# Kernel optimization log

Measured on AMD Instinct MI355X. Metric: run time of the kernel, lower is better.

The kernel has to match this reference:

```python
import jax, jax.numpy as jnp
import numpy as np
from jax import lax

P = 8      # patch size (SGU hard-codes 8x8)
K = 7      # dynamic depthwise kernel size
EPS = 1e-5

def _gelu(x):
    return jax.nn.gelu(x, approximate=False)

def _ln_last(x, w, b):
    mu = jnp.mean(x, -1, keepdims=True)
    var = jnp.var(x, -1, keepdims=True)
    return (x - mu) / jnp.sqrt(var + EPS) * w + b

def _ln_chan(x, w, b):
    # WithBias LayerNorm over channel dim of an NCHW tensor (to_3d/to_4d)
    mu = jnp.mean(x, 1, keepdims=True)
    var = jnp.var(x, 1, keepdims=True)
    return (x - mu) / jnp.sqrt(var + EPS) * w[:, None, None] + b[:, None, None]

def _c1(x, w, b=None):
    # 1x1 conv on NCHW; w: (O, C)
    y = jnp.einsum('bchw,oc->bohw', x, w)
    return y if b is None else y + b[:, None, None]

def _dw3(x, w, b):
    # depthwise 3x3, padding 1; w: (C, 3, 3)
    C = x.shape[1]
    y = lax.conv_general_dilated(x, w[:, None], (1, 1), 'SAME',
        feature_group_count=C, dimension_numbers=('NCHW', 'OIHW', 'NCHW'))
    return y + b[:, None, None]

def _idynamic_dw(x, wdyn):
    # content-adaptive depthwise conv: x (B,C,P,P), per-position kernels
    # wdyn (B,K*K,P,P) shared across channels (groups = C // heads = 1)
    pad = K // 2
    xp = jnp.pad(x, ((0, 0), (0, 0), (pad, pad), (pad, pad)))
    out = jnp.zeros_like(x)
    for k in range(K * K):  # fixed small kernel loop, fused under jit
        i, j = divmod(k, K)
        out = out + xp[:, :, i:i + P, j:j + P] * wdyn[:, k][:, None]
    return out

def _forward(x, w_hid, b_hid, xcnn_w1, xcnn_b1, xcnn_ln_w, xcnn_ln_b,
             xcnn_dw_w, xcnn_dw_b, ci_w1, ci_b1, ci_ln_w, ci_ln_b, ci_w2, ci_b2,
             si_w1, si_b1, si_ln_w, si_ln_b, si_w2, si_b2,
             proj_w, proj_b, out_w, out_b, sgu_ln_w, sgu_ln_b,
             dwb_w0, idw_w1, idw_b1, idw_bn_w, idw_bn_b, idw_w2, idw_b2, dwb_w2):
    b, c, h, w = x.shape
    hh, ww = h // P, w // P
    n = hh * ww
    half = c // 2

    x = _gelu(_c1(x, w_hid, b_hid))
    # b c (hh P)(ww P) -> b hh ww p1 p2 c
    xp = x.reshape(b, c, hh, P, ww, P).transpose(0, 2, 4, 3, 5, 1)
    x_seq = xp.reshape(b, n, P * P, c)

    # x_cnn branch on (b*n, c, 8, 8) patch images
    xc = xp.reshape(b * n, P, P, c).transpose(0, 3, 1, 2)
    xc = _c1(xc, xcnn_w1, xcnn_b1)
    xc = _ln_chan(xc, xcnn_ln_w, xcnn_ln_b)
    xc = _gelu(_dw3(xc, xcnn_dw_w, xcnn_dw_b))

    # channel interaction SE gate -> (b*n, c//2, 1, 1)
    pooled = jnp.mean(xc, (2, 3), keepdims=True)
    cdw = _c1(pooled, ci_w1, ci_b1)
    cdw = _gelu(_ln_chan(cdw, ci_ln_w, ci_ln_b))
    cdw = jax.nn.sigmoid(_c1(cdw, ci_w2, ci_b2))

    # SpatialGatingUnit
    res = x_seq[..., :half].reshape(b * n, P * P, half)
    gate = x_seq[..., half:].reshape(b * n, P * P, half)
    gate = gate * cdw.reshape(b * n, 1, half)
    gate = _ln_last(gate, sgu_ln_w, sgu_ln_b)
    g = gate.reshape(b * n, P, P, half).transpose(0, 3, 1, 2)
    g = _c1(g, dwb_w0)
    # IDynamicDWConv kernel generation (1x1 -> BN(eval, stats 0/1) -> ReLU -> 1x1)
    t = _c1(g, idw_w1, idw_b1)
    t = t / jnp.sqrt(1.0 + EPS) * idw_bn_w[:, None, None] + idw_bn_b[:, None, None]
    t = jax.nn.relu(t)
    wdyn = _c1(t, idw_w2, idw_b2)  # (b*n, K*K, 8, 8)
    g = _idynamic_dw(g, wdyn)
    g = _c1(g, dwb_w2)
    gate = g.transpose(0, 2, 3, 1).reshape(b * n, P * P, half)
    x_sgu = gate * res  # act = Identity

    # stitch patches back to full resolution
    xc_full = xc.reshape(b, hh, ww, c, P, P).transpose(0, 3, 1, 4, 2, 5).reshape(b, c, h, w)
    x_att = x_sgu.reshape(b, hh, ww, P, P, half).transpose(0, 5, 1, 3, 2, 4).reshape(b, half, h, w)

    # spatial interaction gate (b,1,h,w)
    si = _c1(x_att, si_w1, si_b1)
    si = _gelu(_ln_chan(si, si_ln_w, si_ln_b))
    si = jax.nn.sigmoid(_c1(si, si_w2, si_b2))

    xproj = _c1(xc_full, proj_w, proj_b) * si
    out = jnp.concatenate([xproj, x_att], axis=1)
    return _c1(out, out_w, out_b)

def setup_inputs() -> dict:
    key = jax.random.key(0)
    ks = iter(jax.random.split(key, 40))
    dim, half = 64, 32
    B, H, W = 4, 256, 256
    def rn(shape):
        fan_in = int(np.prod(shape[1:])) if len(shape) > 1 else int(shape[0])
        return jax.random.normal(next(ks), shape, jnp.float32) / np.sqrt(fan_in)
    z = lambda n: jnp.zeros((n,), jnp.float32)
    o = lambda n: jnp.ones((n,), jnp.float32)
    return {
        'x': jax.random.normal(next(ks), (B, dim, H, W), jnp.float32),
        'w_hid': rn((dim, dim)), 'b_hid': z(dim),
        'xcnn_w1': rn((dim, dim)), 'xcnn_b1': z(dim),
        'xcnn_ln_w': o(dim), 'xcnn_ln_b': z(dim),
        'xcnn_dw_w': rn((dim, 3, 3)), 'xcnn_dw_b': z(dim),
        'ci_w1': rn((dim // 8, dim)), 'ci_b1': z(dim // 8),
        'ci_ln_w': o(dim // 8), 'ci_ln_b': z(dim // 8),
        'ci_w2': rn((half, dim // 8)), 'ci_b2': z(half),
        'si_w1': rn((dim // 16, half)), 'si_b1': z(dim // 16),
        'si_ln_w': o(dim // 16), 'si_ln_b': z(dim // 16),
        'si_w2': rn((1, dim // 16)), 'si_b2': z(1),
        'proj_w': rn((half, dim)), 'proj_b': z(half),
        'out_w': rn((dim, dim)), 'out_b': z(dim),
        'sgu_ln_w': o(half), 'sgu_ln_b': z(half),
        'dwb_w0': rn((half, half)),
        'idw_w1': rn((half // 4, half)), 'idw_b1': z(half // 4),
        'idw_bn_w': o(half // 4), 'idw_bn_b': z(half // 4),
        'idw_w2': rn((K * K, half // 4)), 'idw_b2': z(K * K),
        'dwb_w2': rn((half, half)),
    }

def reference(x, w_hid, b_hid, xcnn_w1, xcnn_b1, xcnn_ln_w, xcnn_ln_b,
              xcnn_dw_w, xcnn_dw_b, ci_w1, ci_b1, ci_ln_w, ci_ln_b, ci_w2, ci_b2,
              si_w1, si_b1, si_ln_w, si_ln_b, si_w2, si_b2,
              proj_w, proj_b, out_w, out_b, sgu_ln_w, sgu_ln_b,
              dwb_w0, idw_w1, idw_b1, idw_bn_w, idw_bn_b, idw_w2, idw_b2, dwb_w2):
    return _forward(x, w_hid, b_hid, xcnn_w1, xcnn_b1, xcnn_ln_w, xcnn_ln_b,
                    xcnn_dw_w, xcnn_dw_b, ci_w1, ci_b1, ci_ln_w, ci_ln_b, ci_w2, ci_b2,
                    si_w1, si_b1, si_ln_w, si_ln_b, si_w2, si_b2,
                    proj_w, proj_b, out_w, out_b, sgu_ln_w, sgu_ln_b,
                    dwb_w0, idw_w1, idw_b1, idw_bn_w, idw_bn_b, idw_w2, idw_b2, dwb_w2)
```

## Files before the change

kernel.cpp:

```cpp
#include <hip/hip_runtime.h>
#include <math.h>

#define HWSZ 65536
#define EPSF 1e-5f
#define PSTR 4680

typedef __attribute__((ext_vector_type(8))) short bf8v;
typedef __attribute__((ext_vector_type(4))) float f4v;
typedef __attribute__((ext_vector_type(4))) unsigned int u4v;
typedef unsigned int uint32;

#define W_HID_OFF   0
#define W_X1_OFF    4096
#define W_PROJ_OFF  8192
#define W_OUT_OFF   10240
#define W_DWB0_OFF  14336
#define W_DWB2_OFF  15360
#define F_DWT   0
#define F_CI1T  576
#define F_CI2T  1088
#define F_IW1T  1344
#define F_SI1T  1600

__device__ __forceinline__ float sigm(float v){ return 1.0f/(1.0f+expf(-v)); }
__device__ __forceinline__ float bl(uint32 u){ return __uint_as_float(u<<16); }
__device__ __forceinline__ float bh(uint32 u){ return __uint_as_float(u & 0xffff0000u); }
__device__ __forceinline__ uint32 pk2(float a, float b){
  uint32 r; asm("v_cvt_pk_bf16_f32 %0, %1, %2" : "=v"(r) : "v"(a), "v"(b)); return r;
}
__device__ __forceinline__ unsigned short bfr(float x){
  uint32 u = __float_as_uint(x); u += 0x7fffu + ((u>>16)&1u); return (unsigned short)(u>>16);
}
__device__ __forceinline__ float rcp_f(float x){ float r; asm("v_rcp_f32 %0, %1" : "=v"(r) : "v"(x)); return r; }
__device__ __forceinline__ float exp2_f(float x){ float r; asm("v_exp_f32 %0, %1" : "=v"(r) : "v"(x)); return r; }

__device__ __attribute__((noinline)) f4v gelu4(f4v v){
  f4v r;
  #pragma unroll
  for (int i=0;i<4;++i){
    float x  = v[i];
    float z  = fabsf(x) * 0.7071067811865476f;
    float t  = rcp_f(fmaf(0.3275911f, z, 1.0f));
    float p  = t*fmaf(t, fmaf(t, fmaf(t, fmaf(t, 1.061405429f, -1.453152027f),
                       1.421413741f), -0.284496736f), 0.254829592f);
    float ex = exp2_f(-(z*z)*1.4426950408889634f);
    float er = fmaf(-p, ex, 1.0f);
    float s  = copysignf(er, x);
    float hx = 0.5f*x;
    r[i] = fmaf(hx, s, hx);
  }
  return r;
}

#define WSYNC() asm volatile("s_waitcnt lgkmcnt(0)" ::: "memory")

__global__ void prep_w(const float* __restrict__ a0, const float* __restrict__ a1,
                       const float* __restrict__ a2, const float* __restrict__ a3,
                       const float* __restrict__ a4, const float* __restrict__ a5,
                       unsigned short* __restrict__ ws){
  int i = blockIdx.x*256 + threadIdx.x;
  if (i >= 16384) return;
  float v;
  if      (i < 4096)  v = a0[i];
  else if (i < 8192)  v = a1[i-4096];
  else if (i < 10240) v = a2[i-8192];
  else if (i < 14336) v = a3[i-10240];
  else if (i < 15360) v = a4[i-14336];
  else                v = a5[i-15360];
  ws[i] = bfr(v);
}

__global__ void prep_t(const float* __restrict__ dw, const float* __restrict__ ci1,
                       const float* __restrict__ ci2, const float* __restrict__ iw1,
                       const float* __restrict__ sw1, float* __restrict__ wf){
  int i = blockIdx.x*256 + threadIdx.x;
  if (i >= 1728) return;
  float v;
  if (i < 576)        { int k=i/64, c=i%64;            v = dw[c*9+k]; }
  else if (i < 1088)  { int j=i-576,  c=j/8, m=j%8;    v = ci1[m*64+c]; }
  else if (i < 1344)  { int j=i-1088, m=j/32, o=j%32;  v = ci2[o*8+m]; }
  else if (i < 1600)  { int j=i-1344, c=j/8, m=j%8;    v = iw1[m*32+c]; }
  else                { int j=i-1600, c=j/4, m=j%4;    v = sw1[m*32+c]; }
  wf[i] = v;
}

__global__ __launch_bounds__(256, 4)
void gmlp_fused(const float* __restrict__ x,
                const float* __restrict__ b_hid,
                const float* __restrict__ xcnn_b1,
                const float* __restrict__ xcnn_ln_w, const float* __restrict__ xcnn_ln_b,
                const float* __restrict__ xcnn_dw_b,
                const float* __restrict__ ci_b1,
                const float* __restrict__ ci_ln_w, const float* __restrict__ ci_ln_b,
                const float* __restrict__ ci_b2,
                const float* __restrict__ si_b1,
                const float* __restrict__ si_ln_w, const float* __restrict__ si_ln_b,
                const float* __restrict__ si_w2,   const float* __restrict__ si_b2,
                const float* __restrict__ proj_b,
                const float* __restrict__ out_b,
                const float* __restrict__ sgu_ln_w, const float* __restrict__ sgu_ln_b,
                const float* __restrict__ idw_b1,
                const float* __restrict__ idw_bn_w, const float* __restrict__ idw_bn_b,
                const float* __restrict__ idw_w2,  const float* __restrict__ idw_b2,
                const unsigned short* __restrict__ wsw,
                float* __restrict__ out)
{
    __shared__ __align__(16) unsigned short bufS[4*PSTR];
    __shared__ __align__(16) float segate_s[4][32];

    const float* wf = (const float*)wsw + 8192;

    const int tx  = threadIdx.x;
    const int wid = tx >> 6;
    const int t   = tx & 63;
    const int l4  = t & 15, g4 = t >> 4;
    const int py  = t >> 3,  px = t & 7;

    const int bid   = blockIdx.x;
    const int strip = bid & 7;
    const int ph    = (bid >> 3) & 31;
    const int bb    = bid >> 8;

    unsigned short* Wp = bufS + wid*PSTR;

    const int ty  = tx >> 5;
    const int txx = tx & 31;
    const int lp  = txx >> 3;
    const int lpx = txx & 7;
    const int yx  = ty*256 + txx;
    const float* xbase = x + (bb*64)*HWSZ + (ph*8)*256 + strip*32;
    unsigned short* ldst = bufS + lp*PSTR + (ty*8 + lpx)*72;

    #pragma unroll 1
    for (int c8 = 0; c8 < 8; ++c8) {
        u4v w;
        #pragma unroll
        for (int j = 0; j < 4; ++j) {
            int c = c8*8 + 2*j;
            float a = __builtin_nontemporal_load(xbase + c*HWSZ + yx);
            float b = __builtin_nontemporal_load(xbase + (c+1)*HWSZ + yx);
            w[j] = pk2(a, b);
        }
        *(u4v*)(ldst + c8*8) = w;
    }
    if (t < 9) *(u4v*)(Wp + 64*72 + t*8) = (u4v){0,0,0,0};
    __syncthreads();

    f4v acc[4][4];
    #pragma unroll
    for (int m = 0; m < 4; ++m)
        #pragma unroll
        for (int n = 0; n < 4; ++n)
            acc[m][n] = (f4v){0.f,0.f,0.f,0.f};
    #pragma unroll 1
    for (int s = 0; s < 2; ++s) {
        bf8v bw[4]; bf8v av[4];
        #pragma unroll
        for (int n = 0; n < 4; ++n) bw[n] = *(const bf8v*)(wsw + W_HID_OFF + (n*16+l4)*64 + s*32 + g4*8);
        #pragma unroll
        for (int m = 0; m < 4; ++m) av[m] = *(const bf8v*)(Wp + (m*16 + l4)*72 + s*32 + g4*8);
        #pragma unroll
        for (int m = 0; m < 4; ++m)
            #pragma unroll
            for (int n = 0; n < 4; ++n)
                acc[m][n] = __builtin_amdgcn_mfma_f32_16x16x32_bf16(av[m], bw[n], acc[m][n], 0,0,0);
    }
    {
        float bhid[4];
        #pragma unroll
        for (int n = 0; n < 4; ++n) bhid[n] = b_hid[n*16 + l4];
        #pragma unroll
        for (int m = 0; m < 4; ++m)
            #pragma unroll
            for (int n = 0; n < 4; ++n) {
                f4v q;
                #pragma unroll
                for (int r = 0; r < 4; ++r) q[r] = acc[m][n][r] + bhid[n];
                acc[m][n] = gelu4(q);
            }
    }
    WSYNC();
    #pragma unroll
    for (int m = 0; m < 4; ++m)
        #pragma unroll
        for (int n = 0; n < 4; ++n)
            #pragma unroll
            for (int r = 0; r < 4; ++r)
                Wp[(m*16 + g4*4 + r)*72 + n*16 + l4] = bfr(acc[m][n][r]);
    WSYNC();

    uint32 hidpk[32];
    #pragma unroll
    for (int q8 = 0; q8 < 8; ++q8) {
        u4v v = *(const u4v*)(Wp + t*72 + q8*8);
        #pragma unroll
        for (int j = 0; j < 4; ++j) hidpk[q8*4 + j] = v[j];
    }

    #pragma unroll
    for (int m = 0; m < 4; ++m)
        #pragma unroll
        for (int n = 0; n < 4; ++n)
            acc[m][n] = (f4v){0.f,0.f,0.f,0.f};
    #pragma unroll 1
    for (int s = 0; s < 2; ++s) {
        bf8v bw[4]; bf8v av[4];
        #pragma unroll
        for (int n = 0; n < 4; ++n) bw[n] = *(const bf8v*)(wsw + W_X1_OFF + (n*16+l4)*64 + s*32 + g4*8);
        #pragma unroll
        for (int m = 0; m < 4; ++m) av[m] = *(const bf8v*)(Wp + (m*16 + l4)*72 + s*32 + g4*8);
        #pragma unroll
        for (int m = 0; m < 4; ++m)
            #pragma unroll
            for (int n = 0; n < 4; ++n)
                acc[m][n] = __builtin_amdgcn_mfma_f32_16x16x32_bf16(av[m], bw[n], acc[m][n], 0,0,0);
    }
    {
        float bx[4];
        #pragma unroll
        for (int n = 0; n < 4; ++n) bx[n] = xcnn_b1[n*16 + l4];
        #pragma unroll
        for (int m = 0; m < 4; ++m)
            #pragma unroll
            for (int n = 0; n < 4; ++n)
                #pragma unroll
                for (int r = 0; r < 4; ++r)
                    acc[m][n][r] += bx[n];
    }
    WSYNC();
    #pragma unroll
    for (int m = 0; m < 4; ++m)
        #pragma unroll
        for (int n = 0; n < 4; ++n)
            #pragma unroll
            for (int r = 0; r < 4; ++r)
                Wp[(m*16 + g4*4 + r)*72 + n*16 + l4] = bfr(acc[m][n][r]);
    WSYNC();
    {
        float s = 0.f;
        #pragma unroll 1
        for (int q8 = 0; q8 < 8; ++q8) {
            u4v v = *(const u4v*)(Wp + t*72 + q8*8);
            #pragma unroll
            for (int j = 0; j < 4; ++j) s += bl(v[j]) + bh(v[j]);
        }
        float mu = s * (1.f/64.f);
        float s2 = 0.f;
        #pragma unroll 1
        for (int q8 = 0; q8 < 8; ++q8) {
            u4v v = *(const u4v*)(Wp + t*72 + q8*8);
            #pragma unroll
            for (int j = 0; j < 4; ++j) {
                float d0 = bl(v[j]) - mu, d1 = bh(v[j]) - mu;
                s2 = fmaf(d0, d0, fmaf(d1, d1, s2));
            }
        }
        float rstd = rsqrtf(s2*(1.f/64.f) + EPSF);
        #pragma unroll 1
        for (int q8 = 0; q8 < 8; ++q8) {
            u4v v = *(const u4v*)(Wp + t*72 + q8*8);
            u4v w;
            #pragma unroll
            for (int j = 0; j < 4; ++j) {
                int c = q8*8 + 2*j;
                float a = (bl(v[j]) - mu)*rstd*xcnn_ln_w[c]   + xcnn_ln_b[c];
                float b = (bh(v[j]) - mu)*rstd*xcnn_ln_w[c+1] + xcnn_ln_b[c+1];
                w[j] = pk2(a, b);
            }
            *(u4v*)(Wp + t*72 + q8*8) = w;
        }
    }
    WSYNC();

    #pragma unroll 1
    for (int h = 0; h < 2; ++h) {
        float xh[32];
        #pragma unroll
        for (int o = 0; o < 32; ++o) xh[o] = xcnn_dw_b[h*32 + o];
        #pragma unroll 1
        for (int ki = 0; ki < 3; ++ki) {
            #pragma unroll 1
            for (int kj = 0; kj < 3; ++kj) {
                int rr = py + ki - 1, cc = px + kj - 1;
                bool val = ((unsigned)rr < 8u) && ((unsigned)cc < 8u);
                int pnn = val ? rr*8 + cc : 64;
                const unsigned short* rp = Wp + pnn*72 + h*32;
                const float* wp = wf + F_DWT + (ki*3+kj)*64 + h*32;
                #pragma unroll
                for (int c8 = 0; c8 < 4; ++c8) {
                    u4v v = *(const u4v*)(rp + c8*8);
                    #pragma unroll
                    for (int j = 0; j < 4; ++j) {
                        int c = c8*8 + 2*j;
                        xh[c]   = fmaf(bl(v[j]), wp[c],   xh[c]);
                        xh[c+1] = fmaf(bh(v[j]), wp[c+1], xh[c+1]);
                    }
                }
            }
        }
        #pragma unroll
        for (int g = 0; g < 8; ++g) {
            f4v q = (f4v){xh[4*g], xh[4*g+1], xh[4*g+2], xh[4*g+3]};
            q = gelu4(q);
            xh[4*g]=q[0]; xh[4*g+1]=q[1]; xh[4*g+2]=q[2]; xh[4*g+3]=q[3];
        }
        WSYNC();
        #pragma unroll
        for (int c8 = 0; c8 < 4; ++c8) {
            u4v w;
            #pragma unroll
            for (int j = 0; j < 4; ++j) w[j] = pk2(xh[c8*8+2*j], xh[c8*8+2*j+1]);
            *(u4v*)(Wp + t*72 + h*32 + c8*8) = w;
        }
    }
    WSYNC();

    float pc;
    {
        float ps = 0.f;
        #pragma unroll 1
        for (int p8 = 0; p8 < 8; ++p8) {
            #pragma unroll
            for (int q = 0; q < 8; ++q) ps += bl((uint32)Wp[(p8*8+q)*72 + t]);
        }
        pc = ps * (1.f/64.f);
    }
    f4v accp[4][2];
    #pragma unroll
    for (int m = 0; m < 4; ++m) { accp[m][0] = (f4v){0.f,0.f,0.f,0.f}; accp[m][1] = (f4v){0.f,0.f,0.f,0.f}; }
    #pragma unroll 1
    for (int s = 0; s < 2; ++s) {
        bf8v bw[2]; bf8v av[4];
        #pragma unroll
        for (int n = 0; n < 2; ++n) bw[n] = *(const bf8v*)(wsw + W_PROJ_OFF + (n*16+l4)*64 + s*32 + g4*8);
        #pragma unroll
        for (int m = 0; m < 4; ++m) av[m] = *(const bf8v*)(Wp + (m*16 + l4)*72 + s*32 + g4*8);
        #pragma unroll
        for (int m = 0; m < 4; ++m)
            #pragma unroll
            for (int n = 0; n < 2; ++n)
                accp[m][n] = __builtin_amdgcn_mfma_f32_16x16x32_bf16(av[m], bw[n], accp[m][n], 0,0,0);
    }
    {
        float bp0 = proj_b[l4], bp1 = proj_b[16 + l4];
        #pragma unroll
        for (int m = 0; m < 4; ++m)
            #pragma unroll
            for (int r = 0; r < 4; ++r) { accp[m][0][r] += bp0; accp[m][1][r] += bp1; }
    }
    WSYNC();
    #pragma unroll
    for (int m = 0; m < 4; ++m)
        #pragma unroll
        for (int n = 0; n < 2; ++n)
            #pragma unroll
            for (int r = 0; r < 4; ++r)
                Wp[(m*16 + g4*4 + r)*72 + n*16 + l4] = bfr(accp[m][n][r]);
    WSYNC();
    uint32 xppk[16];
    #pragma unroll
    for (int q8 = 0; q8 < 4; ++q8) {
        u4v v = *(const u4v*)(Wp + t*72 + q8*8);
        #pragma unroll
        for (int j = 0; j < 4; ++j) xppk[q8*4 + j] = v[j];
    }

    {
        float pt[8];
        {
            f4v wa = *(const f4v*)(wf + F_CI1T + t*8);
            f4v wb = *(const f4v*)(wf + F_CI1T + t*8 + 4);
            #pragma unroll
            for (int m = 0; m < 4; ++m) { pt[m] = wa[m]*pc; pt[4+m] = wb[m]*pc; }
        }
        #pragma unroll
        for (int st = 1; st < 64; st <<= 1)
            #pragma unroll
            for (int m = 0; m < 8; ++m) pt[m] += __shfl_xor(pt[m], st, 64);
        float t8[8];
        #pragma unroll
        for (int m = 0; m < 8; ++m) t8[m] = pt[m] + ci_b1[m];
        float s = 0.f;
        #pragma unroll
        for (int m = 0; m < 8; ++m) s += t8[m];
        float mu = s * 0.125f;
        float q2 = 0.f;
        #pragma unroll
        for (int m = 0; m < 8; ++m) { float d = t8[m]-mu; q2 = fmaf(d,d,q2); }
        float rstd = rsqrtf(q2*0.125f + EPSF);
        #pragma unroll
        for (int m = 0; m < 8; ++m) t8[m] = (t8[m]-mu)*rstd*ci_ln_w[m] + ci_ln_b[m];
        f4v qa = gelu4((f4v){t8[0],t8[1],t8[2],t8[3]});
        f4v qb = gelu4((f4v){t8[4],t8[5],t8[6],t8[7]});
        t8[0]=qa[0]; t8[1]=qa[1]; t8[2]=qa[2]; t8[3]=qa[3];
        t8[4]=qb[0]; t8[5]=qb[1]; t8[6]=qb[2]; t8[7]=qb[3];
        if (t < 32) {
            float a = ci_b2[t];
            #pragma unroll
            for (int m = 0; m < 8; ++m) a = fmaf(wf[F_CI2T + m*32 + t], t8[m], a);
            segate_s[wid][t] = sigm(a);
        }
    }
    WSYNC();
    float sg[32];
    #pragma unroll
    for (int g = 0; g < 8; ++g) {
        f4v e = *(const f4v*)&segate_s[wid][g*4];
        #pragma unroll
        for (int r = 0; r < 4; ++r) {
            int o = g*4 + r;
            uint32 pkv = hidpk[16 + o/2];
            float gv = (o & 1) ? bh(pkv) : bl(pkv);
            sg[o] = gv * e[r];
        }
    }
    {
        float s = 0.f;
        #pragma unroll
        for (int o = 0; o < 32; ++o) s += sg[o];
        float mu = s * (1.f/32.f);
        float q2 = 0.f;
        #pragma unroll
        for (int o = 0; o < 32; ++o) { float d = sg[o]-mu; q2 = fmaf(d,d,q2); }
        float rstd = rsqrtf(q2*(1.f/32.f) + EPSF);
        #pragma unroll
        for (int o = 0; o < 32; ++o) sg[o] = (sg[o]-mu)*rstd*sgu_ln_w[o] + sgu_ln_b[o];
    }
    WSYNC();
    #pragma unroll
    for (int c8 = 0; c8 < 4; ++c8) {
        u4v w;
        #pragma unroll
        for (int j = 0; j < 4; ++j) w[j] = pk2(sg[c8*8+2*j], sg[c8*8+2*j+1]);
        *(u4v*)(Wp + t*72 + c8*8) = w;
    }
    WSYNC();

    {
        f4v accg[4][2];
        #pragma unroll
        for (int m = 0; m < 4; ++m) { accg[m][0] = (f4v){0.f,0.f,0.f,0.f}; accg[m][1] = (f4v){0.f,0.f,0.f,0.f}; }
        bf8v bw[2]; bf8v av[4];
        #pragma unroll
        for (int n = 0; n < 2; ++n) bw[n] = *(const bf8v*)(wsw + W_DWB0_OFF + (n*16+l4)*32 + g4*8);
        #pragma unroll
        for (int m = 0; m < 4; ++m) av[m] = *(const bf8v*)(Wp + (m*16 + l4)*72 + g4*8);
        #pragma unroll
        for (int m = 0; m < 4; ++m)
            #pragma unroll
            for (int n = 0; n < 2; ++n)
                accg[m][n] = __builtin_amdgcn_mfma_f32_16x16x32_bf16(av[m], bw[n], accg[m][n], 0,0,0);
        WSYNC();
        #pragma unroll
        for (int m = 0; m < 4; ++m)
            #pragma unroll
            for (int n = 0; n < 2; ++n)
                #pragma unroll
                for (int r = 0; r < 4; ++r) {
                    int q = m*16 + g4*4 + r;
                    Wp[((q>>5)*32 + n*16 + l4)*72 + 32 + (q & 31)] = bfr(accg[m][n][r]);
                }
    }
    WSYNC();

    float t8b[8];
    #pragma unroll
    for (int m = 0; m < 8; ++m) t8b[m] = idw_b1[m];
    #pragma unroll 1
    for (int c = 0; c < 32; ++c) {
        float gv = bl((uint32)Wp[((t>>5)*32 + c)*72 + 32 + (t & 31)]);
        #pragma unroll
        for (int m = 0; m < 8; ++m) t8b[m] = fmaf(wf[F_IW1T + c*8 + m], gv, t8b[m]);
    }
    #pragma unroll
    for (int m = 0; m < 8; ++m)
        t8b[m] = fmaxf(t8b[m]*(idw_bn_w[m]*0.9999950000374997f) + idw_bn_b[m], 0.f);

    f4v accd[4][2];
    #pragma unroll
    for (int m = 0; m < 4; ++m) { accd[m][0] = (f4v){0.f,0.f,0.f,0.f}; accd[m][1] = (f4v){0.f,0.f,0.f,0.f}; }
    #pragma unroll 1
    for (int s = 0; s < 2; ++s) {
        WSYNC();
        #pragma unroll
        for (int i = 0; i < 4; ++i) *(u4v*)(Wp + t*72 + i*8) = (u4v){0,0,0,0};
        #pragma unroll 1
        for (int ki = 0; ki < 7; ++ki) {
            int rr = py + ki - 3;
            #pragma unroll 1
            for (int kj = 0; kj < 7; ++kj) {
                int cc = px + kj - 3;
                int k  = ki*7 + kj;
                float wk = idw_b2[k];
                #pragma unroll
                for (int m = 0; m < 8; ++m) wk = fmaf(idw_w2[k*8 + m], t8b[m], wk);
                int q = rr*8 + cc;
                if (((unsigned)rr < 8u) && ((unsigned)cc < 8u) && ((q >> 5) == s))
                    Wp[t*72 + (q & 31)] = bfr(wk);
            }
        }
        WSYNC();
        bf8v aM[4], bG[2];
        #pragma unroll
        for (int m = 0; m < 4; ++m) aM[m] = *(const bf8v*)(Wp + (m*16 + l4)*72 + g4*8);
        #pragma unroll
        for (int n = 0; n < 2; ++n) bG[n] = *(const bf8v*)(Wp + (s*32 + n*16 + l4)*72 + 32 + g4*8);
        #pragma unroll
        for (int m = 0; m < 4; ++m)
            #pragma unroll
            for (int n = 0; n < 2; ++n)
                accd[m][n] = __builtin_amdgcn_mfma_f32_16x16x32_bf16(aM[m], bG[n], accd[m][n], 0,0,0);
    }
    WSYNC();
    #pragma unroll
    for (int m = 0; m < 4; ++m)
        #pragma unroll
        for (int n = 0; n < 2; ++n)
            #pragma unroll
            for (int r = 0; r < 4; ++r)
                Wp[(m*16 + g4*4 + r)*72 + n*16 + l4] = bfr(accd[m][n][r]);
    WSYNC();

    {
        f4v accg[4][2];
        #pragma unroll
        for (int m = 0; m < 4; ++m) { accg[m][0] = (f4v){0.f,0.f,0.f,0.f}; accg[m][1] = (f4v){0.f,0.f,0.f,0.f}; }
        bf8v bw[2]; bf8v av[4];
        #pragma unroll
        for (int n = 0; n < 2; ++n) bw[n] = *(const bf8v*)(wsw + W_DWB2_OFF + (n*16+l4)*32 + g4*8);
        #pragma unroll
        for (int m = 0; m < 4; ++m) av[m] = *(const bf8v*)(Wp + (m*16 + l4)*72 + g4*8);
        #pragma unroll
        for (int m = 0; m < 4; ++m)
            #pragma unroll
            for (int n = 0; n < 2; ++n)
                accg[m][n] = __builtin_amdgcn_mfma_f32_16x16x32_bf16(av[m], bw[n], accg[m][n], 0,0,0);
        WSYNC();
        #pragma unroll
        for (int m = 0; m < 4; ++m)
            #pragma unroll
            for (int n = 0; n < 2; ++n)
                #pragma unroll
                for (int r = 0; r < 4; ++r)
                    Wp[(m*16 + g4*4 + r)*72 + n*16 + l4] = bfr(accg[m][n][r]);
        WSYNC();
    }
    float sgu[32];
    #pragma unroll
    for (int q8 = 0; q8 < 4; ++q8) {
        u4v v = *(const u4v*)(Wp + t*72 + q8*8);
        #pragma unroll
        for (int j = 0; j < 4; ++j) {
            int q = q8*4 + j;
            sgu[2*q]   = bl(v[j]) * bl(hidpk[q]);
            sgu[2*q+1] = bh(v[j]) * bh(hidpk[q]);
        }
    }
    WSYNC();

    #pragma unroll
    for (int c8 = 0; c8 < 4; ++c8) {
        u4v w;
        #pragma unroll
        for (int j = 0; j < 4; ++j) w[j] = pk2(sgu[c8*8+2*j], sgu[c8*8+2*j+1]);
        *(u4v*)(Wp + t*72 + 32 + c8*8) = w;
    }
    WSYNC();
    float siv;
    {
        float s1[4];
        #pragma unroll
        for (int m = 0; m < 4; ++m) s1[m] = si_b1[m];
        #pragma unroll 1
        for (int c8 = 0; c8 < 4; ++c8) {
            u4v v = *(const u4v*)(Wp + t*72 + 32 + c8*8);
            #pragma unroll
            for (int j = 0; j < 4; ++j) {
                int c = c8*8 + 2*j;
                float a0 = bl(v[j]), a1 = bh(v[j]);
                #pragma unroll
                for (int m = 0; m < 4; ++m) {
                    s1[m] = fmaf(wf[F_SI1T + c*4 + m],     a0, s1[m]);
                    s1[m] = fmaf(wf[F_SI1T + (c+1)*4 + m], a1, s1[m]);
                }
            }
        }
        float s = s1[0]+s1[1]+s1[2]+s1[3];
        float mu = s * 0.25f;
        float q2 = 0.f;
        #pragma unroll
        for (int m = 0; m < 4; ++m) { float d = s1[m]-mu; q2 = fmaf(d,d,q2); }
        float rstd = rsqrtf(q2*0.25f + EPSF);
        f4v q;
        #pragma unroll
        for (int m = 0; m < 4; ++m) q[m] = (s1[m]-mu)*rstd*si_ln_w[m] + si_ln_b[m];
        q = gelu4(q);
        float a = si_b2[0];
        #pragma unroll
        for (int m = 0; m < 4; ++m) a = fmaf(si_w2[m], q[m], a);
        siv = sigm(a);
    }
    #pragma unroll
    for (int c8 = 0; c8 < 4; ++c8) {
        u4v w;
        #pragma unroll
        for (int j = 0; j < 4; ++j) {
            int q = c8*4 + j;
            w[j] = pk2(bl(xppk[q])*siv, bh(xppk[q])*siv);
        }
        *(u4v*)(Wp + t*72 + c8*8) = w;
    }
    WSYNC();

    #pragma unroll
    for (int m = 0; m < 4; ++m)
        #pragma unroll
        for (int n = 0; n < 4; ++n)
            acc[m][n] = (f4v){0.f,0.f,0.f,0.f};
    #pragma unroll 1
    for (int s = 0; s < 2; ++s) {
        bf8v bw[4]; bf8v av[4];
        #pragma unroll
        for (int n = 0; n < 4; ++n) bw[n] = *(const bf8v*)(wsw + W_OUT_OFF + (n*16+l4)*64 + s*32 + g4*8);
        #pragma unroll
        for (int m = 0; m < 4; ++m) av[m] = *(const bf8v*)(Wp + (m*16 + l4)*72 + s*32 + g4*8);
        #pragma unroll
        for (int m = 0; m < 4; ++m)
            #pragma unroll
            for (int n = 0; n < 4; ++n)
                acc[m][n] = __builtin_amdgcn_mfma_f32_16x16x32_bf16(av[m], bw[n], acc[m][n], 0,0,0);
    }
    {
        float bo[4];
        #pragma unroll
        for (int n = 0; n < 4; ++n) bo[n] = out_b[n*16 + l4];
        #pragma unroll
        for (int m = 0; m < 4; ++m)
            #pragma unroll
            for (int n = 0; n < 4; ++n)
                #pragma unroll
                for (int r = 0; r < 4; ++r)
                    acc[m][n][r] += bo[n];
    }
    WSYNC();
    #pragma unroll
    for (int m = 0; m < 4; ++m)
        #pragma unroll
        for (int n = 0; n < 4; ++n)
            #pragma unroll
            for (int r = 0; r < 4; ++r)
                Wp[(m*16 + g4*4 + r)*72 + n*16 + l4] = bfr(acc[m][n][r]);
    __syncthreads();

    {
        float* obase = out + (bb*64)*HWSZ + (ph*8)*256 + strip*32;
        const unsigned short* lsrc = bufS + lp*PSTR + (ty*8 + lpx)*72;
        #pragma unroll 1
        for (int c8 = 0; c8 < 8; ++c8) {
            u4v v = *(const u4v*)(lsrc + c8*8);
            #pragma unroll
            for (int j = 0; j < 4; ++j) {
                int c = c8*8 + 2*j;
                __builtin_nontemporal_store(bl(v[j]), obase + c*HWSZ + yx);
                __builtin_nontemporal_store(bh(v[j]), obase + (c+1)*HWSZ + yx);
            }
        }
    }
}

extern "C" void kernel_launch(void* const* d_in, const int* in_sizes, int n_in,
                              void* d_out, int out_size, void* d_ws, size_t ws_size,
                              hipStream_t stream) {
    const float* p[35];
    for (int i = 0; i < 35; ++i) p[i] = (const float*)d_in[i];
    unsigned short* ws = (unsigned short*)d_ws;
    float* wsf = (float*)ws + 8192;

    prep_w<<<64, 256, 0, stream>>>(p[1], p[3], p[21], p[23], p[27], p[34], ws);
    prep_t<<<7, 256, 0, stream>>>(p[7], p[9], p[13], p[28], p[15], wsf);

    const int B = in_sizes[0] / (64 * 256 * 256);
    dim3 grid(B * 32 * 8), block(256);
    gmlp_fused<<<grid, block, 0, stream>>>(
        p[0],  p[2],  p[4],  p[5],  p[6],  p[8],
        p[10], p[11], p[12], p[14],
        p[16], p[17], p[18], p[19], p[20],
        p[22], p[24], p[25], p[26],
        p[29], p[30], p[31], p[32], p[33],
        ws, (float*)d_out);
}
```

Before: 96.72 us.

## Split each 8x8 patch across two waves, halving patches per block

Before, each wave processed one whole patch (four patches per 256-thread block). Now each block handles two patches, with two waves per patch, and each wave computes half the output channels of every GEMM and depthwise stage. The grid doubles, LDS per block halves and the launch-bounds occupancy hint rises from 4 to 5. This is meant to cut per-wave register pressure and serial work so latency hides better. The cost is many more block-wide __syncthreads (replacing wave-local waitcnt), some stages running on one wave only, and narrower global loads. Sigmoid is also switched to a hardware exp2/rcp approximation.

```diff
diff --git a/kernel.cpp b/kernel.cpp
--- a/kernel.cpp
+++ b/kernel.cpp
@@ -8,6 +8,7 @@
 typedef __attribute__((ext_vector_type(8))) short bf8v;
 typedef __attribute__((ext_vector_type(4))) float f4v;
 typedef __attribute__((ext_vector_type(4))) unsigned int u4v;
+typedef __attribute__((ext_vector_type(2))) unsigned int u2v;
 typedef unsigned int uint32;
 
 #define W_HID_OFF   0
@@ -22,7 +23,6 @@
 #define F_IW1T  1344
 #define F_SI1T  1600
 
-__device__ __forceinline__ float sigm(float v){ return 1.0f/(1.0f+expf(-v)); }
 __device__ __forceinline__ float bl(uint32 u){ return __uint_as_float(u<<16); }
 __device__ __forceinline__ float bh(uint32 u){ return __uint_as_float(u & 0xffff0000u); }
 __device__ __forceinline__ uint32 pk2(float a, float b){
@@ -33,6 +33,9 @@
 }
 __device__ __forceinline__ float rcp_f(float x){ float r; asm("v_rcp_f32 %0, %1" : "=v"(r) : "v"(x)); return r; }
 __device__ __forceinline__ float exp2_f(float x){ float r; asm("v_exp_f32 %0, %1" : "=v"(r) : "v"(x)); return r; }
+__device__ __forceinline__ float sigm(float v){
+  return rcp_f(1.0f + exp2_f(v * -1.4426950408889634f));
+}
 
 __device__ __attribute__((noinline)) f4v gelu4(f4v v){
   f4v r;
@@ -52,8 +55,6 @@
   return r;
 }
 
-#define WSYNC() asm volatile("s_waitcnt lgkmcnt(0)" ::: "memory")
-
 __global__ void prep_w(const float* __restrict__ a0, const float* __restrict__ a1,
                        const float* __restrict__ a2, const float* __restrict__ a3,
                        const float* __restrict__ a4, const float* __restrict__ a5,
@@ -84,7 +85,7 @@
   wf[i] = v;
 }
 
-__global__ __launch_bounds__(256, 4)
+__global__ __launch_bounds__(256, 5)
 void gmlp_fused(const float* __restrict__ x,
                 const float* __restrict__ b_hid,
                 const float* __restrict__ xcnn_b1,
@@ -105,137 +106,136 @@
                 const unsigned short* __restrict__ wsw,
                 float* __restrict__ out)
 {
-    __shared__ __align__(16) unsigned short bufS[4*PSTR];
-    __shared__ __align__(16) float segate_s[4][32];
+    __shared__ __align__(16) unsigned short bufS[2*PSTR];
+    __shared__ __align__(16) float segate_s[2][32];
 
     const float* wf = (const float*)wsw + 8192;
 
     const int tx  = threadIdx.x;
-    const int wid = tx >> 6;
+    const int wp_ = tx >> 7;
+    const int wv  = (tx >> 6) & 1;
     const int t   = tx & 63;
     const int l4  = t & 15, g4 = t >> 4;
     const int py  = t >> 3,  px = t & 7;
 
-    const int bid   = blockIdx.x;
-    const int strip = bid & 7;
-    const int ph    = (bid >> 3) & 31;
-    const int bb    = bid >> 8;
-
-    unsigned short* Wp = bufS + wid*PSTR;
-
-    const int ty  = tx >> 5;
-    const int txx = tx & 31;
+    const int bid = blockIdx.x;
+    const int s16 = bid & 15;
+    const int ph  = (bid >> 4) & 31;
+    const int bb  = bid >> 9;
+
+    unsigned short* Wp = bufS + wp_*PSTR;
+
+    const int ch2 = tx >> 7;
+    const int r128 = tx & 127;
+    const int ty  = r128 >> 4;
+    const int txx = r128 & 15;
     const int lp  = txx >> 3;
     const int lpx = txx & 7;
     const int yx  = ty*256 + txx;
-    const float* xbase = x + (bb*64)*HWSZ + (ph*8)*256 + strip*32;
-    unsigned short* ldst = bufS + lp*PSTR + (ty*8 + lpx)*72;
+    const float* xbase = x + (bb*64)*HWSZ + (ph*8)*256 + s16*16;
+    unsigned short* ldst = bufS + lp*PSTR + (ty*8 + lpx)*72 + ch2*4;
 
     #pragma unroll 1
     for (int c8 = 0; c8 < 8; ++c8) {
-        u4v w;
-        #pragma unroll
-        for (int j = 0; j < 4; ++j) {
-            int c = c8*8 + 2*j;
-            float a = __builtin_nontemporal_load(xbase + c*HWSZ + yx);
-            float b = __builtin_nontemporal_load(xbase + (c+1)*HWSZ + yx);
-            w[j] = pk2(a, b);
-        }
-        *(u4v*)(ldst + c8*8) = w;
-    }
-    if (t < 9) *(u4v*)(Wp + 64*72 + t*8) = (u4v){0,0,0,0};
-    __syncthreads();
-
-    f4v acc[4][4];
+        int c = c8*8 + ch2*4;
+        u2v w;
+        w[0] = pk2(__builtin_nontemporal_load(xbase + c*HWSZ + yx),
+                   __builtin_nontemporal_load(xbase + (c+1)*HWSZ + yx));
+        w[1] = pk2(__builtin_nontemporal_load(xbase + (c+2)*HWSZ + yx),
+                   __builtin_nontemporal_load(xbase + (c+3)*HWSZ + yx));
+        *(u2v*)(ldst + c8*8) = w;
+    }
+    if (tx < 18) *(u4v*)(bufS + (tx/9)*PSTR + 64*72 + (tx%9)*8) = (u4v){0,0,0,0};
+    __syncthreads();
+
+    f4v acc[4][2];
+    #pragma unroll
+    for (int m = 0; m < 4; ++m) { acc[m][0] = (f4v){0,0,0,0}; acc[m][1] = (f4v){0,0,0,0}; }
+    {
+        bf8v a0[4], a1[4], w0[2], w1[2];
+        #pragma unroll
+        for (int nn = 0; nn < 2; ++nn) {
+            w0[nn] = *(const bf8v*)(wsw + W_HID_OFF + ((wv*2+nn)*16+l4)*64 + g4*8);
+            w1[nn] = *(const bf8v*)(wsw + W_HID_OFF + ((wv*2+nn)*16+l4)*64 + 32 + g4*8);
+        }
+        #pragma unroll
+        for (int m = 0; m < 4; ++m) a0[m] = *(const bf8v*)(Wp + (m*16+l4)*72 + g4*8);
+        #pragma unroll
+        for (int m = 0; m < 4; ++m) a1[m] = *(const bf8v*)(Wp + (m*16+l4)*72 + 32 + g4*8);
+        #pragma unroll
+        for (int m = 0; m < 4; ++m)
+            #pragma unroll
+            for (int nn = 0; nn < 2; ++nn) {
+                acc[m][nn] = __builtin_amdgcn_mfma_f32_16x16x32_bf16(a0[m], w0[nn], acc[m][nn], 0,0,0);
+                acc[m][nn] = __builtin_amdgcn_mfma_f32_16x16x32_bf16(a1[m], w1[nn], acc[m][nn], 0,0,0);
+            }
+    }
+    {
+        float bh0 = b_hid[(wv*2)*16 + l4], bh1 = b_hid[(wv*2+1)*16 + l4];
+        #pragma unroll
+        for (int m = 0; m < 4; ++m) {
+            f4v q0, q1;
+            #pragma unroll
+            for (int r = 0; r < 4; ++r) { q0[r] = acc[m][0][r] + bh0; q1[r] = acc[m][1][r] + bh1; }
+            acc[m][0] = gelu4(q0); acc[m][1] = gelu4(q1);
+        }
+    }
+    __syncthreads();
     #pragma unroll
     for (int m = 0; m < 4; ++m)
         #pragma unroll
-        for (int n = 0; n < 4; ++n)
-            acc[m][n] = (f4v){0.f,0.f,0.f,0.f};
-    #pragma unroll 1
-    for (int s = 0; s < 2; ++s) {
-        bf8v bw[4]; bf8v av[4];
-        #pragma unroll
-        for (int n = 0; n < 4; ++n) bw[n] = *(const bf8v*)(wsw + W_HID_OFF + (n*16+l4)*64 + s*32 + g4*8);
-        #pragma unroll
-        for (int m = 0; m < 4; ++m) av[m] = *(const bf8v*)(Wp + (m*16 + l4)*72 + s*32 + g4*8);
-        #pragma unroll
-        for (int m = 0; m < 4; ++m)
-            #pragma unroll
-            for (int n = 0; n < 4; ++n)
-                acc[m][n] = __builtin_amdgcn_mfma_f32_16x16x32_bf16(av[m], bw[n], acc[m][n], 0,0,0);
-    }
-    {
-        float bhid[4];
-        #pragma unroll
-        for (int n = 0; n < 4; ++n) bhid[n] = b_hid[n*16 + l4];
-        #pragma unroll
-        for (int m = 0; m < 4; ++m)
-            #pragma unroll
-            for (int n = 0; n < 4; ++n) {
-                f4v q;
-                #pragma unroll
-                for (int r = 0; r < 4; ++r) q[r] = acc[m][n][r] + bhid[n];
-                acc[m][n] = gelu4(q);
-            }
-    }
-    WSYNC();
+        for (int nn = 0; nn < 2; ++nn)
+            #pragma unroll
+            for (int r = 0; r < 4; ++r)
+                Wp[(m*16 + g4*4 + r)*72 + (wv*2+nn)*16 + l4] = bfr(acc[m][nn][r]);
+    __syncthreads();
+
+    uint32 hpk[16];
+    #pragma unroll
+    for (int q4 = 0; q4 < 4; ++q4) {
+        u4v v = *(const u4v*)(Wp + t*72 + wv*32 + q4*8);
+        #pragma unroll
+        for (int j = 0; j < 4; ++j) hpk[q4*4 + j] = v[j];
+    }
+
+    #pragma unroll
+    for (int m = 0; m < 4; ++m) { acc[m][0] = (f4v){0,0,0,0}; acc[m][1] = (f4v){0,0,0,0}; }
+    {
+        bf8v a0[4], a1[4], w0[2], w1[2];
+        #pragma unroll
+        for (int nn = 0; nn < 2; ++nn) {
+            w0[nn] = *(const bf8v*)(wsw + W_X1_OFF + ((wv*2+nn)*16+l4)*64 + g4*8);
+            w1[nn] = *(const bf8v*)(wsw + W_X1_OFF + ((wv*2+nn)*16+l4)*64 + 32 + g4*8);
+        }
+        #pragma unroll
+        for (int m = 0; m < 4; ++m) a0[m] = *(const bf8v*)(Wp + (m*16+l4)*72 + g4*8);
+        #pragma unroll
+        for (int m = 0; m < 4; ++m) a1[m] = *(const bf8v*)(Wp + (m*16+l4)*72 + 32 + g4*8);
+        #pragma unroll
+        for (int m = 0; m < 4; ++m)
+            #pragma unroll
+            for (int nn = 0; nn < 2; ++nn) {
+                acc[m][nn] = __builtin_amdgcn_mfma_f32_16x16x32_bf16(a0[m], w0[nn], acc[m][nn], 0,0,0);
+                acc[m][nn] = __builtin_amdgcn_mfma_f32_16x16x32_bf16(a1[m], w1[nn], acc[m][nn], 0,0,0);
+            }
+    }
+    {
+        float bx0 = xcnn_b1[(wv*2)*16 + l4], bx1 = xcnn_b1[(wv*2+1)*16 + l4];
+        #pragma unroll
+        for (int m = 0; m < 4; ++m)
+            #pragma unroll
+            for (int r = 0; r < 4; ++r) { acc[m][0][r] += bx0; acc[m][1][r] += bx1; }
+    }
+    __syncthreads();
     #pragma unroll
     for (int m = 0; m < 4; ++m)
         #pragma unroll
-        for (int n = 0; n < 4; ++n)
+        for (int nn = 0; nn < 2; ++nn)
             #pragma unroll
             for (int r = 0; r < 4; ++r)
-                Wp[(m*16 + g4*4 + r)*72 + n*16 + l4] = bfr(acc[m][n][r]);
-    WSYNC();
-
-    uint32 hidpk[32];
-    #pragma unroll
-    for (int q8 = 0; q8 < 8; ++q8) {
-        u4v v = *(const u4v*)(Wp + t*72 + q8*8);
-        #pragma unroll
-        for (int j = 0; j < 4; ++j) hidpk[q8*4 + j] = v[j];
-    }
-
-    #pragma unroll
-    for (int m = 0; m < 4; ++m)
-        #pragma unroll
-        for (int n = 0; n < 4; ++n)
-            acc[m][n] = (f4v){0.f,0.f,0.f,0.f};
-    #pragma unroll 1
-    for (int s = 0; s < 2; ++s) {
-        bf8v bw[4]; bf8v av[4];
-        #pragma unroll
-        for (int n = 0; n < 4; ++n) bw[n] = *(const bf8v*)(wsw + W_X1_OFF + (n*16+l4)*64 + s*32 + g4*8);
-        #pragma unroll
-        for (int m = 0; m < 4; ++m) av[m] = *(const bf8v*)(Wp + (m*16 + l4)*72 + s*32 + g4*8);
-        #pragma unroll
-        for (int m = 0; m < 4; ++m)
-            #pragma unroll
-            for (int n = 0; n < 4; ++n)
-                acc[m][n] = __builtin_amdgcn_mfma_f32_16x16x32_bf16(av[m], bw[n], acc[m][n], 0,0,0);
-    }
-    {
-        float bx[4];
-        #pragma unroll
-        for (int n = 0; n < 4; ++n) bx[n] = xcnn_b1[n*16 + l4];
-        #pragma unroll
-        for (int m = 0; m < 4; ++m)
-            #pragma unroll
-            for (int n = 0; n < 4; ++n)
-                #pragma unroll
-                for (int r = 0; r < 4; ++r)
-                    acc[m][n][r] += bx[n];
-    }
-    WSYNC();
-    #pragma unroll
-    for (int m = 0; m < 4; ++m)
-        #pragma unroll
-        for (int n = 0; n < 4; ++n)
-            #pragma unroll
-            for (int r = 0; r < 4; ++r)
-                Wp[(m*16 + g4*4 + r)*72 + n*16 + l4] = bfr(acc[m][n][r]);
-    WSYNC();
+                Wp[(m*16 + g4*4 + r)*72 + (wv*2+nn)*16 + l4] = bfr(acc[m][nn][r]);
+    __syncthreads();
+
     {
         float s = 0.f;
         #pragma unroll 1
@@ -256,8 +256,9 @@
             }
         }
         float rstd = rsqrtf(s2*(1.f/64.f) + EPSF);
+        __syncthreads();
         #pragma unroll 1
-        for (int q8 = 0; q8 < 8; ++q8) {
+        for (int q8 = wv*4; q8 < wv*4 + 4; ++q8) {
             u4v v = *(const u4v*)(Wp + t*72 + q8*8);
             u4v w;
             #pragma unroll
@@ -270,13 +271,12 @@
             *(u4v*)(Wp + t*72 + q8*8) = w;
         }
     }
-    WSYNC();
-
-    #pragma unroll 1
-    for (int h = 0; h < 2; ++h) {
+    __syncthreads();
+
+    {
         float xh[32];
         #pragma unroll
-        for (int o = 0; o < 32; ++o) xh[o] = xcnn_dw_b[h*32 + o];
+        for (int o = 0; o < 32; ++o) xh[o] = xcnn_dw_b[wv*32 + o];
         #pragma unroll 1
         for (int ki = 0; ki < 3; ++ki) {
             #pragma unroll 1
@@ -284,16 +284,16 @@
                 int rr = py + ki - 1, cc = px + kj - 1;
                 bool val = ((unsigned)rr < 8u) && ((unsigned)cc < 8u);
                 int pnn = val ? rr*8 + cc : 64;
-                const unsigned short* rp = Wp + pnn*72 + h*32;
-                const float* wp = wf + F_DWT + (ki*3+kj)*64 + h*32;
+                const unsigned short* rp = Wp + pnn*72 + wv*32;
+                const float* wpt = wf + F_DWT + (ki*3+kj)*64 + wv*32;
                 #pragma unroll
                 for (int c8 = 0; c8 < 4; ++c8) {
                     u4v v = *(const u4v*)(rp + c8*8);
                     #pragma unroll
                     for (int j = 0; j < 4; ++j) {
                         int c = c8*8 + 2*j;
-                        xh[c]   = fmaf(bl(v[j]), wp[c],   xh[c]);
-                        xh[c+1] = fmaf(bh(v[j]), wp[c+1], xh[c+1]);
+                        xh[c]   = fmaf(bl(v[j]), wpt[c],   xh[c]);
+                        xh[c+1] = fmaf(bh(v[j]), wpt[c+1], xh[c+1]);
                     }
                 }
             }
@@ -304,19 +304,18 @@
             q = gelu4(q);
             xh[4*g]=q[0]; xh[4*g+1]=q[1]; xh[4*g+2]=q[2]; xh[4*g+3]=q[3];
         }
-        WSYNC();
         #pragma unroll
         for (int c8 = 0; c8 < 4; ++c8) {
             u4v w;
             #pragma unroll
             for (int j = 0; j < 4; ++j) w[j] = pk2(xh[c8*8+2*j], xh[c8*8+2*j+1]);
-            *(u4v*)(Wp + t*72 + h*32 + c8*8) = w;
-        }
-    }
-    WSYNC();
-
-    float pc;
-    {
+            *(u4v*)(Wp + t*72 + wv*32 + c8*8) = w;
+        }
+    }
+    __syncthreads();
+
+    float pc = 0.f;
+    if (wv == 1) {
         float ps = 0.f;
         #pragma unroll 1
         for (int p8 = 0; p8 < 8; ++p8) {
@@ -325,47 +324,47 @@
         }
         pc = ps * (1.f/64.f);
     }
-    f4v accp[4][2];
-    #pragma unroll
-    for (int m = 0; m < 4; ++m) { accp[m][0] = (f4v){0.f,0.f,0.f,0.f}; accp[m][1] = (f4v){0.f,0.f,0.f,0.f}; }
-    #pragma unroll 1
-    for (int s = 0; s < 2; ++s) {
-        bf8v bw[2]; bf8v av[4];
-        #pragma unroll
-        for (int n = 0; n < 2; ++n) bw[n] = *(const bf8v*)(wsw + W_PROJ_OFF + (n*16+l4)*64 + s*32 + g4*8);
-        #pragma unroll
-        for (int m = 0; m < 4; ++m) av[m] = *(const bf8v*)(Wp + (m*16 + l4)*72 + s*32 + g4*8);
-        #pragma unroll
-        for (int m = 0; m < 4; ++m)
-            #pragma unroll
-            for (int n = 0; n < 2; ++n)
-                accp[m][n] = __builtin_amdgcn_mfma_f32_16x16x32_bf16(av[m], bw[n], accp[m][n], 0,0,0);
-    }
-    {
-        float bp0 = proj_b[l4], bp1 = proj_b[16 + l4];
-        #pragma unroll
-        for (int m = 0; m < 4; ++m)
-            #pragma unroll
-            for (int r = 0; r < 4; ++r) { accp[m][0][r] += bp0; accp[m][1][r] += bp1; }
-    }
-    WSYNC();
+    f4v accp[4];
+    #pragma unroll
+    for (int m = 0; m < 4; ++m) accp[m] = (f4v){0,0,0,0};
+    {
+        bf8v a0[4], a1[4], w0, w1;
+        w0 = *(const bf8v*)(wsw + W_PROJ_OFF + (wv*16+l4)*64 + g4*8);
+        w1 = *(const bf8v*)(wsw + W_PROJ_OFF + (wv*16+l4)*64 + 32 + g4*8);
+        #pragma unroll
+        for (int m = 0; m < 4; ++m) a0[m] = *(const bf8v*)(Wp + (m*16+l4)*72 + g4*8);
+        #pragma unroll
+        for (int m = 0; m < 4; ++m) a1[m] = *(const bf8v*)(Wp + (m*16+l4)*72 + 32 + g4*8);
+        #pragma unroll
+        for (int m = 0; m < 4; ++m) {
+            accp[m] = __builtin_amdgcn_mfma_f32_16x16x32_bf16(a0[m], w0, accp[m], 0,0,0);
+            accp[m] = __builtin_amdgcn_mfma_f32_16x16x32_bf16(a1[m], w1, accp[m], 0,0,0);
+        }
+    }
+    {
+        float bp = proj_b[wv*16 + l4];
+        #pragma unroll
+        for (int m = 0; m < 4; ++m)
+            #pragma unroll
+            for (int r = 0; r < 4; ++r) accp[m][r] += bp;
+    }
+    __syncthreads();
     #pragma unroll
     for (int m = 0; m < 4; ++m)
         #pragma unroll
-        for (int n = 0; n < 2; ++n)
-            #pragma unroll
-            for (int r = 0; r < 4; ++r)
-                Wp[(m*16 + g4*4 + r)*72 + n*16 + l4] = bfr(accp[m][n][r]);
-    WSYNC();
-    uint32 xppk[16];
-    #pragma unroll
-    for (int q8 = 0; q8 < 4; ++q8) {
-        u4v v = *(const u4v*)(Wp + t*72 + q8*8);
-        #pragma unroll
-        for (int j = 0; j < 4; ++j) xppk[q8*4 + j] = v[j];
-    }
-
-    {
+        for (int r = 0; r < 4; ++r)
+            Wp[(m*16 + g4*4 + r)*72 + wv*16 + l4] = bfr(accp[m][r]);
+    __syncthreads();
+    uint32 xppk8[8];
+    #pragma unroll
+    for (int q4 = 0; q4 < 2; ++q4) {
+        u4v v = *(const u4v*)(Wp + t*72 + wv*16 + q4*8);
+        #pragma unroll
+        for (int j = 0; j < 4; ++j) xppk8[q4*4 + j] = v[j];
+    }
+    __syncthreads();
+
+    if (wv == 1) {
         float pt[8];
         {
             f4v wa = *(const f4v*)(wf + F_CI1T + t*8);
@@ -398,70 +397,60 @@
             float a = ci_b2[t];
             #pragma unroll
             for (int m = 0; m < 8; ++m) a = fmaf(wf[F_CI2T + m*32 + t], t8[m], a);
-            segate_s[wid][t] = sigm(a);
-        }
-    }
-    WSYNC();
-    float sg[32];
-    #pragma unroll
-    for (int g = 0; g < 8; ++g) {
-        f4v e = *(const f4v*)&segate_s[wid][g*4];
-        #pragma unroll
-        for (int r = 0; r < 4; ++r) {
-            int o = g*4 + r;
-            uint32 pkv = hidpk[16 + o/2];
-            float gv = (o & 1) ? bh(pkv) : bl(pkv);
-            sg[o] = gv * e[r];
-        }
-    }
-    {
-        float s = 0.f;
-        #pragma unroll
-        for (int o = 0; o < 32; ++o) s += sg[o];
-        float mu = s * (1.f/32.f);
-        float q2 = 0.f;
-        #pragma unroll
-        for (int o = 0; o < 32; ++o) { float d = sg[o]-mu; q2 = fmaf(d,d,q2); }
-        float rstd = rsqrtf(q2*(1.f/32.f) + EPSF);
-        #pragma unroll
-        for (int o = 0; o < 32; ++o) sg[o] = (sg[o]-mu)*rstd*sgu_ln_w[o] + sgu_ln_b[o];
-    }
-    WSYNC();
-    #pragma unroll
-    for (int c8 = 0; c8 < 4; ++c8) {
-        u4v w;
-        #pragma unroll
-        for (int j = 0; j < 4; ++j) w[j] = pk2(sg[c8*8+2*j], sg[c8*8+2*j+1]);
-        *(u4v*)(Wp + t*72 + c8*8) = w;
-    }
-    WSYNC();
-
-    {
-        f4v accg[4][2];
-        #pragma unroll
-        for (int m = 0; m < 4; ++m) { accg[m][0] = (f4v){0.f,0.f,0.f,0.f}; accg[m][1] = (f4v){0.f,0.f,0.f,0.f}; }
-        bf8v bw[2]; bf8v av[4];
-        #pragma unroll
-        for (int n = 0; n < 2; ++n) bw[n] = *(const bf8v*)(wsw + W_DWB0_OFF + (n*16+l4)*32 + g4*8);
-        #pragma unroll
-        for (int m = 0; m < 4; ++m) av[m] = *(const bf8v*)(Wp + (m*16 + l4)*72 + g4*8);
-        #pragma unroll
-        for (int m = 0; m < 4; ++m)
-            #pragma unroll
-            for (int n = 0; n < 2; ++n)
-                accg[m][n] = __builtin_amdgcn_mfma_f32_16x16x32_bf16(av[m], bw[n], accg[m][n], 0,0,0);
-        WSYNC();
-        #pragma unroll
-        for (int m = 0; m < 4; ++m)
-            #pragma unroll
-            for (int n = 0; n < 2; ++n)
-                #pragma unroll
-                for (int r = 0; r < 4; ++r) {
-                    int q = m*16 + g4*4 + r;
-                    Wp[((q>>5)*32 + n*16 + l4)*72 + 32 + (q & 31)] = bfr(accg[m][n][r]);
-                }
-    }
-    WSYNC();
+            segate_s[wp_][t] = sigm(a);
+        }
+        float sg[32];
+        #pragma unroll
+        for (int g = 0; g < 8; ++g) {
+            f4v e = *(const f4v*)&segate_s[wp_][g*4];
+            #pragma unroll
+            for (int r = 0; r < 4; ++r) {
+                int o = g*4 + r;
+                uint32 pkv = hpk[o/2];
+                float gv = (o & 1) ? bh(pkv) : bl(pkv);
+                sg[o] = gv * e[r];
+            }
+        }
+        float ss = 0.f;
+        #pragma unroll
+        for (int o = 0; o < 32; ++o) ss += sg[o];
+        float mu2 = ss * (1.f/32.f);
+        float qq = 0.f;
+        #pragma unroll
+        for (int o = 0; o < 32; ++o) { float d = sg[o]-mu2; qq = fmaf(d,d,qq); }
+        float rstd2 = rsqrtf(qq*(1.f/32.f) + EPSF);
+        #pragma unroll
+        for (int o = 0; o < 32; ++o) sg[o] = (sg[o]-mu2)*rstd2*sgu_ln_w[o] + sgu_ln_b[o];
+        #pragma unroll
+        for (int c8 = 0; c8 < 4; ++c8) {
+            u4v w;
+            #pragma unroll
+            for (int j = 0; j < 4; ++j) w[j] = pk2(sg[c8*8+2*j], sg[c8*8+2*j+1]);
+            *(u4v*)(Wp + t*72 + c8*8) = w;
+        }
+    }
+    __syncthreads();
+
+    {
+        f4v accg[4];
+        #pragma unroll
+        for (int m = 0; m < 4; ++m) accg[m] = (f4v){0,0,0,0};
+        bf8v av[4];
+        bf8v w0 = *(const bf8v*)(wsw + W_DWB0_OFF + (wv*16+l4)*32 + g4*8);
+        #pragma unroll
+        for (int m = 0; m < 4; ++m) av[m] = *(const bf8v*)(Wp + (m*16+l4)*72 + g4*8);
+        #pragma unroll
+        for (int m = 0; m < 4; ++m)
+            accg[m] = __builtin_amdgcn_mfma_f32_16x16x32_bf16(av[m], w0, accg[m], 0,0,0);
+        #pragma unroll
+        for (int m = 0; m < 4; ++m)
+            #pragma unroll
+            for (int r = 0; r < 4; ++r) {
+                int q = m*16 + g4*4 + r;
+                Wp[((q>>5)*32 + wv*16 + l4)*72 + 32 + (q & 31)] = bfr(accg[m][r]);
+            }
+    }
+    __syncthreads();
 
     float t8b[8];
     #pragma unroll
@@ -476,96 +465,81 @@
     for (int m = 0; m < 8; ++m)
         t8b[m] = fmaxf(t8b[m]*(idw_bn_w[m]*0.9999950000374997f) + idw_bn_b[m], 0.f);
 
-    f4v accd[4][2];
-    #pragma unroll
-    for (int m = 0; m < 4; ++m) { accd[m][0] = (f4v){0.f,0.f,0.f,0.f}; accd[m][1] = (f4v){0.f,0.f,0.f,0.f}; }
+    f4v accd[4];
+    #pragma unroll
+    for (int m = 0; m < 4; ++m) accd[m] = (f4v){0,0,0,0};
     #pragma unroll 1
     for (int s = 0; s < 2; ++s) {
-        WSYNC();
-        #pragma unroll
-        for (int i = 0; i < 4; ++i) *(u4v*)(Wp + t*72 + i*8) = (u4v){0,0,0,0};
-        #pragma unroll 1
-        for (int ki = 0; ki < 7; ++ki) {
-            int rr = py + ki - 3;
+        if (wv == s) {
+            #pragma unroll
+            for (int i = 0; i < 4; ++i) *(u4v*)(Wp + t*72 + i*8) = (u4v){0,0,0,0};
             #pragma unroll 1
-            for (int kj = 0; kj < 7; ++kj) {
-                int cc = px + kj - 3;
-                int k  = ki*7 + kj;
-                float wk = idw_b2[k];
-                #pragma unroll
-                for (int m = 0; m < 8; ++m) wk = fmaf(idw_w2[k*8 + m], t8b[m], wk);
-                int q = rr*8 + cc;
-                if (((unsigned)rr < 8u) && ((unsigned)cc < 8u) && ((q >> 5) == s))
-                    Wp[t*72 + (q & 31)] = bfr(wk);
-            }
-        }
-        WSYNC();
-        bf8v aM[4], bG[2];
-        #pragma unroll
-        for (int m = 0; m < 4; ++m) aM[m] = *(const bf8v*)(Wp + (m*16 + l4)*72 + g4*8);
-        #pragma unroll
-        for (int n = 0; n < 2; ++n) bG[n] = *(const bf8v*)(Wp + (s*32 + n*16 + l4)*72 + 32 + g4*8);
-        #pragma unroll
-        for (int m = 0; m < 4; ++m)
-            #pragma unroll
-            for (int n = 0; n < 2; ++n)
-                accd[m][n] = __builtin_amdgcn_mfma_f32_16x16x32_bf16(aM[m], bG[n], accd[m][n], 0,0,0);
-    }
-    WSYNC();
+            for (int ki = 0; ki < 7; ++ki) {
+                int rr = py + ki - 3;
+                #pragma unroll 1
+                for (int kj = 0; kj < 7; ++kj) {
+                    int cc = px + kj - 3;
+                    int k  = ki*7 + kj;
+                    float wk = idw_b2[k];
+                    #pragma unroll
+                    for (int m = 0; m < 8; ++m) wk = fmaf(idw_w2[k*8 + m], t8b[m], wk);
+                    int q = rr*8 + cc;
+                    if (((unsigned)rr < 8u) && ((unsigned)cc < 8u) && ((q >> 5) == s))
+                        Wp[t*72 + (q & 31)] = bfr(wk);
+                }
+            }
+        }
+        __syncthreads();
+        bf8v aM[4];
+        bf8v bG = *(const bf8v*)(Wp + (s*32 + wv*16 + l4)*72 + 32 + g4*8);
+        #pragma unroll
+        for (int m = 0; m < 4; ++m) aM[m] = *(const bf8v*)(Wp + (m*16+l4)*72 + g4*8);
+        #pragma unroll
+        for (int m = 0; m < 4; ++m)
+            accd[m] = __builtin_amdgcn_mfma_f32_16x16x32_bf16(aM[m], bG, accd[m], 0,0,0);
+        __syncthreads();
+    }
     #pragma unroll
     for (int m = 0; m < 4; ++m)
         #pragma unroll
-        for (int n = 0; n < 2; ++n)
+        for (int r = 0; r < 4; ++r)
+            Wp[(m*16 + g4*4 + r)*72 + wv*16 + l4] = bfr(accd[m][r]);
+    __syncthreads();
+
+    {
+        f4v accg[4];
+        #pragma unroll
+        for (int m = 0; m < 4; ++m) accg[m] = (f4v){0,0,0,0};
+        bf8v av[4];
+        bf8v w0 = *(const bf8v*)(wsw + W_DWB2_OFF + (wv*16+l4)*32 + g4*8);
+        #pragma unroll
+        for (int m = 0; m < 4; ++m) av[m] = *(const bf8v*)(Wp + (m*16+l4)*72 + g4*8);
+        #pragma unroll
+        for (int m = 0; m < 4; ++m)
+            accg[m] = __builtin_amdgcn_mfma_f32_16x16x32_bf16(av[m], w0, accg[m], 0,0,0);
+        __syncthreads();
+        #pragma unroll
+        for (int m = 0; m < 4; ++m)
             #pragma unroll
             for (int r = 0; r < 4; ++r)
-                Wp[(m*16 + g4*4 + r)*72 + n*16 + l4] = bfr(accd[m][n][r]);
-    WSYNC();
-
-    {
-        f4v accg[4][2];
-        #pragma unroll
-        for (int m = 0; m < 4; ++m) { accg[m][0] = (f4v){0.f,0.f,0.f,0.f}; accg[m][1] = (f4v){0.f,0.f,0.f,0.f}; }
-        bf8v bw[2]; bf8v av[4];
-        #pragma unroll
-        for (int n = 0; n < 2; ++n) bw[n] = *(const bf8v*)(wsw + W_DWB2_OFF + (n*16+l4)*32 + g4*8);
-        #pragma unroll
-        for (int m = 0; m < 4; ++m) av[m] = *(const bf8v*)(Wp + (m*16 + l4)*72 + g4*8);
-        #pragma unroll
-        for (int m = 0; m < 4; ++m)
-            #pragma unroll
-            for (int n = 0; n < 2; ++n)
-                accg[m][n] = __builtin_amdgcn_mfma_f32_16x16x32_bf16(av[m], bw[n], accg[m][n], 0,0,0);
-        WSYNC();
-        #pragma unroll
-        for (int m = 0; m < 4; ++m)
-            #pragma unroll
-            for (int n = 0; n < 2; ++n)
-                #pragma unroll
-                for (int r = 0; r < 4; ++r)
-                    Wp[(m*16 + g4*4 + r)*72 + n*16 + l4] = bfr(accg[m][n][r]);
-        WSYNC();
-    }
-    float sgu[32];
-    #pragma unroll
-    for (int q8 = 0; q8 < 4; ++q8) {
-        u4v v = *(const u4v*)(Wp + t*72 + q8*8);
-        #pragma unroll
-        for (int j = 0; j < 4; ++j) {
-            int q = q8*4 + j;
-            sgu[2*q]   = bl(v[j]) * bl(hidpk[q]);
-            sgu[2*q+1] = bh(v[j]) * bh(hidpk[q]);
-        }
-    }
-    WSYNC();
-
-    #pragma unroll
-    for (int c8 = 0; c8 < 4; ++c8) {
-        u4v w;
-        #pragma unroll
-        for (int j = 0; j < 4; ++j) w[j] = pk2(sgu[c8*8+2*j], sgu[c8*8+2*j+1]);
-        *(u4v*)(Wp + t*72 + 32 + c8*8) = w;
-    }
-    WSYNC();
+                Wp[(m*16 + g4*4 + r)*72 + wv*16 + l4] = bfr(accg[m][r]);
+    }
+    __syncthreads();
+    if (wv == 0) {
+        #pragma unroll
+        for (int q8 = 0; q8 < 4; ++q8) {
+            u4v v = *(const u4v*)(Wp + t*72 + q8*8);
+            u4v w;
+            #pragma unroll
+            for (int j = 0; j < 4; ++j) {
+                int q = q8*4 + j;
+                w[j] = pk2(bl(v[j]) * bl(hpk[q]), bh(v[j]) * bh(hpk[q]));
+            }
+            *(u4v*)(Wp + t*72 + 32 + q8*8) = w;
+        }
+    }
+    __syncthreads();
+
     float siv;
     {
         float s1[4];
@@ -601,69 +575,66 @@
         siv = sigm(a);
     }
     #pragma unroll
-    for (int c8 = 0; c8 < 4; ++c8) {
+    for (int c4 = 0; c4 < 2; ++c4) {
         u4v w;
         #pragma unroll
         for (int j = 0; j < 4; ++j) {
-            int q = c8*4 + j;
-            w[j] = pk2(bl(xppk[q])*siv, bh(xppk[q])*siv);
-        }
-        *(u4v*)(Wp + t*72 + c8*8) = w;
-    }
-    WSYNC();
-
+            int q = c4*4 + j;
+            w[j] = pk2(bl(xppk8[q])*siv, bh(xppk8[q])*siv);
+        }
+        *(u4v*)(Wp + t*72 + wv*16 + c4*8) = w;
+    }
+    __syncthreads();
+
+    #pragma unroll
+    for (int m = 0; m < 4; ++m) { acc[m][0] = (f4v){0,0,0,0}; acc[m][1] = (f4v){0,0,0,0}; }
+    {
+        bf8v a0[4], a1[4], w0[2], w1[2];
+        #pragma unroll
+        for (int nn = 0; nn < 2; ++nn) {
+            w0[nn] = *(const bf8v*)(wsw + W_OUT_OFF + ((wv*2+nn)*16+l4)*64 + g4*8);
+            w1[nn] = *(const bf8v*)(wsw + W_OUT_OFF + ((wv*2+nn)*16+l4)*64 + 32 + g4*8);
+        }
+        #pragma unroll
+        for (int m = 0; m < 4; ++m) a0[m] = *(const bf8v*)(Wp + (m*16+l4)*72 + g4*8);
+        #pragma unroll
+        for (int m = 0; m < 4; ++m) a1[m] = *(const bf8v*)(Wp + (m*16+l4)*72 + 32 + g4*8);
+        #pragma unroll
+        for (int m = 0; m < 4; ++m)
+            #pragma unroll
+            for (int nn = 0; nn < 2; ++nn) {
+                acc[m][nn] = __builtin_amdgcn_mfma_f32_16x16x32_bf16(a0[m], w0[nn], acc[m][nn], 0,0,0);
+                acc[m][nn] = __builtin_amdgcn_mfma_f32_16x16x32_bf16(a1[m], w1[nn], acc[m][nn], 0,0,0);
+            }
+    }
+    {
+        float bo0 = out_b[(wv*2)*16 + l4], bo1 = out_b[(wv*2+1)*16 + l4];
+        #pragma unroll
+        for (int m = 0; m < 4; ++m)
+            #pragma unroll
+            for (int r = 0; r < 4; ++r) { acc[m][0][r] += bo0; acc[m][1][r] += bo1; }
+    }
+    __syncthreads();
     #pragma unroll
     for (int m = 0; m < 4; ++m)
         #pragma unroll
-        for (int n = 0; n < 4; ++n)
-            acc[m][n] = (f4v){0.f,0.f,0.f,0.f};
-    #pragma unroll 1
-    for (int s = 0; s < 2; ++s) {
-        bf8v bw[4]; bf8v av[4];
-        #pragma unroll
-        for (int n = 0; n < 4; ++n) bw[n] = *(const bf8v*)(wsw + W_OUT_OFF + (n*16+l4)*64 + s*32 + g4*8);
-        #pragma unroll
-        for (int m = 0; m < 4; ++m) av[m] = *(const bf8v*)(Wp + (m*16 + l4)*72 + s*32 + g4*8);
-        #pragma unroll
-        for (int m = 0; m < 4; ++m)
-            #pragma unroll
-            for (int n = 0; n < 4; ++n)
-                acc[m][n] = __builtin_amdgcn_mfma_f32_16x16x32_bf16(av[m], bw[n], acc[m][n], 0,0,0);
-    }
-    {
-        float bo[4];
-        #pragma unroll
-        for (int n = 0; n < 4; ++n) bo[n] = out_b[n*16 + l4];
-        #pragma unroll
-        for (int m = 0; m < 4; ++m)
-            #pragma unroll
-            for (int n = 0; n < 4; ++n)
-                #pragma unroll
-                for (int r = 0; r < 4; ++r)
-                    acc[m][n][r] += bo[n];
-    }
-    WSYNC();
-    #pragma unroll
-    for (int m = 0; m < 4; ++m)
-        #pragma unroll
-        for (int n = 0; n < 4; ++n)
+        for (int nn = 0; nn < 2; ++nn)
             #pragma unroll
             for (int r = 0; r < 4; ++r)
-                Wp[(m*16 + g4*4 + r)*72 + n*16 + l4] = bfr(acc[m][n][r]);
-    __syncthreads();
-
-    {
-        float* obase = out + (bb*64)*HWSZ + (ph*8)*256 + strip*32;
-        const unsigned short* lsrc = bufS + lp*PSTR + (ty*8 + lpx)*72;
+                Wp[(m*16 + g4*4 + r)*72 + (wv*2+nn)*16 + l4] = bfr(acc[m][nn][r]);
+    __syncthreads();
+
+    {
+        float* obase = out + (bb*64)*HWSZ + (ph*8)*256 + s16*16;
+        const unsigned short* lsrc = bufS + lp*PSTR + (ty*8 + lpx)*72 + ch2*4;
         #pragma unroll 1
         for (int c8 = 0; c8 < 8; ++c8) {
-            u4v v = *(const u4v*)(lsrc + c8*8);
-            #pragma unroll
-            for (int j = 0; j < 4; ++j) {
-                int c = c8*8 + 2*j;
-                __builtin_nontemporal_store(bl(v[j]), obase + c*HWSZ + yx);
-                __builtin_nontemporal_store(bh(v[j]), obase + (c+1)*HWSZ + yx);
-            }
+            int c = c8*8 + ch2*4;
+            u2v v = *(const u2v*)(lsrc + c8*8);
+            __builtin_nontemporal_store(bl(v[0]), obase + c*HWSZ + yx);
+            __builtin_nontemporal_store(bh(v[0]), obase + (c+1)*HWSZ + yx);
+            __builtin_nontemporal_store(bl(v[1]), obase + (c+2)*HWSZ + yx);
+            __builtin_nontemporal_store(bh(v[1]), obase + (c+3)*HWSZ + yx);
         }
     }
 }
@@ -680,7 +651,7 @@
     prep_t<<<7, 256, 0, stream>>>(p[7], p[9], p[13], p[28], p[15], wsf);
 
     const int B = in_sizes[0] / (64 * 256 * 256);
-    dim3 grid(B * 32 * 8), block(256);
+    dim3 grid(B * 32 * 16), block(256);
     gmlp_fused<<<grid, block, 0, stream>>>(
         p[0],  p[2],  p[4],  p[5],  p[6],  p[8],
         p[10], p[11], p[12], p[14],
```

After: 143.4 us. 48.2% more time.
